# Kernel optimization log

Measured on AMD Instinct MI355X. Metric: run time of the kernel, lower is better.

## Reference

```python
import jax, jax.numpy as jnp
import numpy as np

HIDDEN = 100


def _mlp(x, w1, b1, w2, b2):
    # MLP(in, HIDDEN, output_size=out): Linear -> ReLU -> Linear
    return jnp.maximum(x @ w1 + b1, 0.0) @ w2 + b2


def _row_norm_mean(d):
    # mean_i sqrt(sum_j d_ij^2)  == torch.sqrt(einsum('ij,ij->i')).mean()
    return jnp.sqrt(jnp.einsum('ij,ij->i', d, d)).mean()


def _mismatch_1nn(mapped, target, idx):
    # torch_mapping_misclassified_1nn: cdist(mapped[idx], target), top-1 NN,
    # count non-integer distances at mismatched rows / len(idx).
    a = mapped[idx]                                     # [K, d]
    d2 = (jnp.sum(a * a, axis=1, keepdims=True)
          + jnp.sum(target * target, axis=1)[None, :]
          - 2.0 * a @ target.T)                         # [K, N]
    dist = jnp.sqrt(jnp.maximum(d2, 0.0))
    vals = jnp.min(dist, axis=1)                        # top-1 smallest value
    nn_inds = jnp.argmin(dist, axis=1)
    mismatch = (nn_inds != idx)
    count = (jnp.ceil(vals) - jnp.floor(vals)) * mismatch.astype(vals.dtype)
    return count.sum() / idx.shape[0]


def setup_inputs() -> dict:
    key = jax.random.key(0)
    ks = jax.random.split(key, 8)
    xN, yN, xd, yd, K = 25000, 25000, 100, 120, 8000
    s = 0.1
    return {
        'x_weight': jax.random.normal(ks[0], (xN, xd), jnp.float32) * s,
        'y_weight': jax.random.normal(ks[1], (yN, yd), jnp.float32) * s,
        'fx_w1': jax.random.normal(ks[2], (xd, HIDDEN), jnp.float32) * (1.0 / np.sqrt(xd)),
        'fx_b1': jnp.zeros((HIDDEN,), jnp.float32),
        'fx_w2': jax.random.normal(ks[3], (HIDDEN, yd), jnp.float32) * (1.0 / np.sqrt(HIDDEN)),
        'fx_b2': jnp.zeros((yd,), jnp.float32),
        'gy_w1': jax.random.normal(ks[4], (yd, HIDDEN), jnp.float32) * (1.0 / np.sqrt(yd)),
        'gy_b1': jnp.zeros((HIDDEN,), jnp.float32),
        'gy_w2': jax.random.normal(ks[5], (HIDDEN, xd), jnp.float32) * (1.0 / np.sqrt(HIDDEN)),
        'gy_b2': jnp.zeros((xd,), jnp.float32),
        'index_map': jax.random.randint(ks[6], (K, 2), 0, min(xN, yN), jnp.int64 if jax.config.jax_enable_x64 else jnp.int32),
    }


def reference(x_weight, y_weight, fx_w1, fx_b1, fx_w2, fx_b2,
              gy_w1, gy_b1, gy_w2, gy_b2, index_map):
    x_mapped = _mlp(x_weight, fx_w1, fx_b1, fx_w2, fx_b2)   # fx(x_emb)  [xN, yd]
    y_mapped = _mlp(y_weight, gy_w1, gy_b1, gy_w2, gy_b2)   # gy(y_emb)  [yN, xd]

    # cycle losses
    x_rt = _mlp(x_mapped, gy_w1, gy_b1, gy_w2, gy_b2)
    cycle_fx = _row_norm_mean(x_rt - x_weight)
    y_rt = _mlp(y_mapped, fx_w1, fx_b1, fx_w2, fx_b2)
    cycle_gy = _row_norm_mean(y_rt - y_weight)

    x_intersect = index_map[:, 0]
    y_intersect = index_map[:, 1]

    # supervised alignment losses
    sup_x = _row_norm_mean(x_mapped[x_intersect] - y_weight[y_intersect])
    sup_y = _row_norm_mean(y_mapped[y_intersect] - x_weight[x_intersect])

    # 1-NN mismatch losses (the cdist + top-1 hot spots)
    fx_mismatch = _mismatch_1nn(x_mapped, y_weight, x_intersect)
    gy_mismatch = _mismatch_1nn(y_mapped, x_weight, y_intersect)

    return cycle_fx + cycle_gy + sup_x + fx_mismatch + sup_y + gy_mismatch
```

## Files before the change

### kernel.cpp

```cpp
#include <hip/hip_runtime.h>
#include <hip/hip_bf16.h>
#include <math.h>

#define HIDDEN 100

typedef __attribute__((ext_vector_type(8))) short bf16x8;
typedef __attribute__((ext_vector_type(4))) float f32x4;

__device__ inline unsigned short f2bf(float v) {
    union { float f; unsigned u; } x; x.f = v;
    unsigned r = x.u + 0x7fff + ((x.u >> 16) & 1);
    return (unsigned short)(r >> 16);
}

constexpr int NPTS  = 25000;
constexpr int KPAIR = 8000;
constexpr int NC    = 28;
constexpr int CHUNK = 896;
constexpr int NPAD  = NC * CHUNK;
constexpr int HS    = 136;
constexpr int NB_SUP = 2000;
constexpr int GM     = (NPTS + 31) / 32;
constexpr int NB_MLP = 2 * GM;
constexpr int PREP_B = (2 * NPAD) / 4;

__global__ __launch_bounds__(256) void prep_kernel(
    const float* __restrict__ YW, float* __restrict__ tny, unsigned short* __restrict__ ybf,
    const float* __restrict__ XW, float* __restrict__ tnx, unsigned short* __restrict__ xbf,
    const float* __restrict__ W1, unsigned short* __restrict__ P1,
    const float* __restrict__ W2, unsigned short* __restrict__ P2,
    const float* __restrict__ W3, unsigned short* __restrict__ P3,
    const float* __restrict__ W4, unsigned short* __restrict__ P4,
    int N)
{
    const int ln = threadIdx.x & 63;
    if (blockIdx.x < PREP_B) {
        const int gw = blockIdx.x * 4 + (threadIdx.x >> 6);
        const int isY = (gw < NPAD);
        const int r = isY ? gw : gw - NPAD;
        const int D = isY ? 120 : 100;
        unsigned short* dst = (isY ? ybf : xbf) + (size_t)r * 128;
        if (r < N) {
            const float* src = (isY ? YW : XW) + (size_t)r * D;
            const float v0 = (ln < D) ? src[ln] : 0.f;
            const float v1 = (ln + 64 < D) ? src[ln + 64] : 0.f;
            float s = fmaf(v0, v0, v1 * v1);
            #pragma unroll
            for (int o = 1; o < 64; o <<= 1) s += __shfl_xor(s, o);
            if (ln == 0) (isY ? tny : tnx)[r] = s;
            dst[ln] = f2bf(v0);
            dst[ln + 64] = (ln == 63) ? f2bf(s) : f2bf(v1);
        } else {
            dst[ln] = 0;
            dst[ln + 64] = (ln == 63) ? f2bf(1e30f) : (unsigned short)0;
        }
        return;
    }
    int b = (blockIdx.x - PREP_B) * 4 + (threadIdx.x >> 6);
    if (b >= 116) return;
    const float* W; unsigned short* P; int DK, DN, NT;
    if (b < 28)      {          W = W1; P = P1; DK = 100; DN = 100; NT = 7; }
    else if (b < 60) { b -= 28; W = W2; P = P2; DK = 100; DN = 120; NT = 8; }
    else if (b < 88) { b -= 60; W = W3; P = P3; DK = 120; DN = 100; NT = 7; }
    else             { b -= 88; W = W4; P = P4; DK = 100; DN = 100; NT = 7; }
    const int kt = b / NT, nt = b - kt * NT;
    const int n  = nt * 16 + (ln & 15);
    const int k0 = kt * 32 + (ln >> 4) * 8;
    unsigned short* dst = P + ((size_t)(kt * NT + nt) * 64 + ln) * 8;
    #pragma unroll
    for (int j = 0; j < 8; j++) {
        const int k = k0 + j;
        const float f = (k < DK && n < DN) ? W[k * DN + n] : 0.f;
        dst[j] = f2bf(f);
    }
}

template<int NT>
__device__ inline void run_stage(const bf16x8 af[4], const unsigned short* __restrict__ WP,
                                 int ln, f32x4 acc[NT])
{
    #pragma unroll
    for (int nt = 0; nt < NT; nt++) acc[nt] = (f32x4){0.f, 0.f, 0.f, 0.f};
    #pragma unroll
    for (int kt = 0; kt < 4; kt++) {
        #pragma unroll
        for (int nt = 0; nt < NT; nt++) {
            const bf16x8 wf = *reinterpret_cast<const bf16x8*>(WP + ((size_t)(kt * NT + nt) * 64 + ln) * 8);
            acc[nt] = __builtin_amdgcn_mfma_f32_16x16x32_bf16(af[kt], wf, acc[nt], 0, 0, 0);
        }
    }
}

template<int NT, int DN, bool RELU>
__device__ inline void pack_h(const f32x4 acc[NT], const float* __restrict__ B,
                              unsigned short* __restrict__ Hs, int col, int quad)
{
    #pragma unroll
    for (int nt = 0; nt < NT; nt++) {
        const int n = nt * 16 + col;
        const float b = (n < DN) ? B[n] : 0.f;
        #pragma unroll
        for (int r = 0; r < 4; r++) {
            float v = acc[nt][r] + b;
            if (RELU) v = fmaxf(v, 0.f);
            Hs[(quad * 4 + r) * HS + n] = f2bf(v);
        }
    }
}

template<int NT, int DN>
__device__ inline void store_pack(const f32x4 acc[NT], const float* __restrict__ B,
                                  float* __restrict__ Y, unsigned short* __restrict__ Hs,
                                  int rowbase, int col, int quad, int N)
{
    #pragma unroll
    for (int nt = 0; nt < NT; nt++) {
        const int n = nt * 16 + col;
        const float b = (n < DN) ? B[n] : 0.f;
        #pragma unroll
        for (int r = 0; r < 4; r++) {
            const float v = acc[nt][r] + b;
            const int row = rowbase + quad * 4 + r;
            if (n < DN && row < N) Y[(size_t)row * DN + n] = v;
            Hs[(quad * 4 + r) * HS + n] = f2bf(v);
        }
    }
}

__device__ inline void load_haf(const unsigned short* __restrict__ Hs, int col, int quad,
                                bf16x8 af[4])
{
    const unsigned short* p = Hs + col * HS + quad * 8;
    #pragma unroll
    for (int kt = 0; kt < 4; kt++)
        af[kt] = *reinterpret_cast<const bf16x8*>(p + kt * 32);
}

template<int NT, int DN>
__device__ inline float norm_stage(const f32x4 acc[NT], const float* __restrict__ B,
                                   const float* __restrict__ REF,
                                   int rowbase, int col, int quad, int N)
{
    float ra[4] = {0.f, 0.f, 0.f, 0.f};
    #pragma unroll
    for (int nt = 0; nt < NT; nt++) {
        const int n = nt * 16 + col;
        if (n < DN) {
            const float b = B[n];
            #pragma unroll
            for (int r = 0; r < 4; r++) {
                const int row = rowbase + quad * 4 + r;
                if (row < N) {
                    const float d = acc[nt][r] + b - REF[(size_t)row * DN + n];
                    ra[r] = fmaf(d, d, ra[r]);
                }
            }
        }
    }
    #pragma unroll
    for (int o = 1; o < 16; o <<= 1) {
        #pragma unroll
        for (int r = 0; r < 4; r++) ra[r] += __shfl_xor(ra[r], o);
    }
    float s = 0.f;
    if (col == 0) {
        #pragma unroll
        for (int r = 0; r < 4; r++)
            if (rowbase + quad * 4 + r < N) s += sqrtf(ra[r]);
    }
    return s;
}

template<int DIN, int DMID, int NT2, int NTF>
__global__ __launch_bounds__(128) void mlp_fused(
    const unsigned short* __restrict__ Xbf,
    const float* __restrict__ XREF,
    const unsigned short* __restrict__ WP1, const float* __restrict__ B1,
    const unsigned short* __restrict__ WP2, const float* __restrict__ B2,
    const unsigned short* __restrict__ WP3, const float* __restrict__ B3,
    const unsigned short* __restrict__ WP4, const float* __restrict__ B4,
    float* __restrict__ Y,
    float* __restrict__ part, int N)
{
    __shared__ unsigned short H[2][16 * HS];
    __shared__ float bred[8];

    const int tid = threadIdx.x;
    const int wv = tid >> 6, ln = tid & 63;
    const int col = ln & 15, quad = ln >> 4;
    const int rowbase = blockIdx.x * 32 + wv * 16;

    {
        unsigned* Hz = reinterpret_cast<unsigned*>(H[wv]);
        for (int i = ln; i < 16 * HS / 2; i += 64) Hz[i] = 0u;
    }

    bf16x8 af[4];
    {
        const int r = min(rowbase + col, N - 1);
        const unsigned short* ap = Xbf + (size_t)r * 128 + quad * 8;
        #pragma unroll
        for (int kt = 0; kt < 4; kt++) af[kt] = *reinterpret_cast<const bf16x8*>(ap + kt * 32);
    }

    f32x4 accA[7];
    run_stage<7>(af, WP1, ln, accA);
    pack_h<7, HIDDEN, true>(accA, B1, H[wv], col, quad);
    load_haf(H[wv], col, quad, af);

    f32x4 accB[NT2];
    run_stage<NT2>(af, WP2, ln, accB);
    store_pack<NT2, DMID>(accB, B2, Y, H[wv], rowbase, col, quad, N);
    load_haf(H[wv], col, quad, af);

    run_stage<7>(af, WP3, ln, accA);
    pack_h<7, HIDDEN, true>(accA, B3, H[wv], col, quad);
    load_haf(H[wv], col, quad, af);

    f32x4 accC[NTF];
    run_stage<NTF>(af, WP4, ln, accC);
    const float s = norm_stage<NTF, DIN>(accC, B4, XREF, rowbase, col, quad, N);

    if (col == 0) bred[wv * 4 + quad] = s;
    __syncthreads();
    if (tid == 0) {
        float t = 0.f;
        #pragma unroll
        for (int i = 0; i < 8; i++) t += bred[i];
        part[blockIdx.x] = t;
    }
}

__global__ __launch_bounds__(256) void sup_gather(
    const float* __restrict__ xm, const float* __restrict__ ym,
    const float* __restrict__ xw, const float* __restrict__ yw,
    const int* __restrict__ im, int K, float* __restrict__ part,
    unsigned short* __restrict__ axf, unsigned short* __restrict__ ayf)
{
    const int gw = (int)((blockIdx.x * 256 + threadIdx.x) >> 6);
    const int ln = threadIdx.x & 63;
    const int wv = threadIdx.x >> 6;
    float cnt = 0.f;
    if (gw < K) {
        const int xi = im[2 * gw], yi = im[2 * gw + 1];
        const float* a = xm + (size_t)xi * 120;
        const float* b = yw + (size_t)yi * 120;
        const float a0 = a[ln];
        const float a1 = (ln + 64 < 120) ? a[ln + 64] : 0.f;
        float s1 = 0.f;
        { const float d0 = a0 - b[ln]; s1 = d0 * d0; }
        if (ln + 64 < 120) { const float d1 = a1 - b[ln + 64]; s1 = fmaf(d1, d1, s1); }
        unsigned short* pax = axf + (size_t)gw * 128;
        pax[ln] = f2bf(-2.f * a0);
        pax[ln + 64] = (ln == 63) ? f2bf(1.f) : ((ln + 64 < 120) ? f2bf(-2.f * a1) : (unsigned short)0);

        const float* c = ym + (size_t)yi * 100;
        const float* e = xw + (size_t)xi * 100;
        const float c0 = c[ln];
        const float c1 = (ln + 64 < 100) ? c[ln + 64] : 0.f;
        float s2 = 0.f;
        { const float d0 = c0 - e[ln]; s2 = d0 * d0; }
        if (ln + 64 < 100) { const float d1 = c1 - e[ln + 64]; s2 = fmaf(d1, d1, s2); }
        unsigned short* pay = ayf + (size_t)gw * 128;
        pay[ln] = f2bf(-2.f * c0);
        pay[ln + 64] = (ln == 63) ? f2bf(1.f) : ((ln + 64 < 100) ? f2bf(-2.f * c1) : (unsigned short)0);

        #pragma unroll
        for (int o = 32; o > 0; o >>= 1) { s1 += __shfl_down(s1, o); s2 += __shfl_down(s2, o); }
        if (ln == 0) cnt = sqrtf(s1) + sqrtf(s2);
    }
    __shared__ float wsum[4];
    if (ln == 0) wsum[wv] = cnt;
    __syncthreads();
    if (threadIdx.x == 0)
        part[blockIdx.x] = wsum[0] + wsum[1] + wsum[2] + wsum[3];
}

__device__ inline void stage_tile(const unsigned short* __restrict__ T, int jbase,
                                  unsigned char* smem, int buf, int wv, int ln)
{
    #pragma unroll
    for (int h = 0; h < 2; h++) {
        const int c = h * 256 + wv * 64 + ln;
        const int r = c >> 4;
        const int gc = (c & 15) ^ (r & 15);
        const unsigned short* g = T + ((size_t)(jbase + r) << 7) + gc * 8;
        unsigned char* l = smem + buf * 8192 + h * 4096 + wv * 1024;
        __builtin_amdgcn_global_load_lds(
            (const __attribute__((address_space(1))) void*)g,
            (__attribute__((address_space(3))) void*)l, 16, 0, 0);
    }
}

__global__ __launch_bounds__(256, 3) void nn_mfma(
    const unsigned short* __restrict__ A0, const unsigned short* __restrict__ T0,
    float* __restrict__ pm0, int* __restrict__ pi0,
    const unsigned short* __restrict__ A1, const unsigned short* __restrict__ T1,
    float* __restrict__ pm1, int* __restrict__ pi1,
    int K)
{
    __shared__ __align__(16) unsigned char smem[17408];
    float (*rm)[64][17] = reinterpret_cast<float(*)[64][17]>(smem);

    const unsigned short* A = blockIdx.z ? A1 : A0;
    const unsigned short* T = blockIdx.z ? T1 : T0;
    float* pmin = blockIdx.z ? pm1 : pm0;
    int*   pidx = blockIdx.z ? pi1 : pi0;

    const int tid = threadIdx.x;
    const int wv = tid >> 6, ln = tid & 63;
    const int col = ln & 15, quad = ln >> 4;
    const int k0 = blockIdx.x * 256;
    const int jstart = blockIdx.y * CHUNK;
    constexpr int NTILES = CHUNK / 32;

    bf16x8 afrag[4][4];
    #pragma unroll
    for (int t = 0; t < 4; t++) {
        const int ar = min(k0 + wv * 64 + t * 16 + col, K - 1);
        const unsigned short* ab = A + (size_t)ar * 128 + quad * 8;
        #pragma unroll
        for (int s = 0; s < 4; s++)
            afrag[t][s] = *reinterpret_cast<const bf16x8*>(ab + s * 32);
    }

    float m[4][4];
    #pragma unroll
    for (int t = 0; t < 4; t++)
        #pragma unroll
        for (int r = 0; r < 4; r++) m[t][r] = __builtin_inff();

    stage_tile(T, jstart, smem, 0, wv, ln);
    __syncthreads();

    for (int ti = 0; ti < NTILES; ti++) {
        const int cur = ti & 1;
        if (ti + 1 < NTILES)
            stage_tile(T, jstart + (ti + 1) * 32, smem, cur ^ 1, wv, ln);

        const unsigned short* base = (const unsigned short*)(smem + cur * 8192);
        const unsigned lowbase = (unsigned)((jstart + ti * 32) >> 4);
        #pragma unroll
        for (int sub = 0; sub < 2; sub++) {
            bf16x8 bfr[4];
            const int rr = sub * 16 + col;
            #pragma unroll
            for (int s = 0; s < 4; s++) {
                const int ch = rr * 16 + ((quad + s * 4) ^ col);
                bfr[s] = *reinterpret_cast<const bf16x8*>(base + ch * 8);
            }
            const unsigned low = lowbase + sub;
            #pragma unroll
            for (int t = 0; t < 4; t++) {
                f32x4 acc = {0.f, 0.f, 0.f, 0.f};
                #pragma unroll
                for (int s = 0; s < 4; s++)
                    acc = __builtin_amdgcn_mfma_f32_16x16x32_bf16(afrag[t][s], bfr[s], acc, 0, 0, 0);
                #pragma unroll
                for (int r = 0; r < 4; r++) {
                    const unsigned u = (__float_as_uint(acc[r]) & 0xFFFFF800u) | low;
                    m[t][r] = fminf(m[t][r], __uint_as_float(u));
                }
            }
        }
        __syncthreads();
    }

    #pragma unroll
    for (int t = 0; t < 4; t++)
        #pragma unroll
        for (int r = 0; r < 4; r++)
            rm[wv][t * 16 + quad * 4 + r][col] = m[t][r];
    __syncthreads();

    const int k = k0 + tid;
    if (k < K) {
        const int w = tid >> 6, rr = tid & 63;
        float best = rm[w][rr][0];
        int bc = 0;
        #pragma unroll
        for (int c = 1; c < 16; c++) {
            const float v = rm[w][rr][c];
            if (v < best) { best = v; bc = c; }
        }
        const int j = (int)(((__float_as_uint(best) & 0x7FFu) << 4) | (unsigned)bc);
        pmin[(size_t)k * NC + blockIdx.y] = best;
        pidx[(size_t)k * NC + blockIdx.y] = j;
    }
}

__global__ __launch_bounds__(256) void finish_all(
    const int* __restrict__ im,
    const float* __restrict__ pm0, const int* __restrict__ pi0,
    const float* __restrict__ pm1, const int* __restrict__ pi1,
    const float* __restrict__ part_sup, const float* __restrict__ part_mlp,
    int K, float* __restrict__ out, float inv_k, float inv_n)
{
    const int gid = blockIdx.x * 256 + threadIdx.x;
    const int stride = gridDim.x * 256;
    float local = 0.f;

    for (int p = gid; p < 2 * K; p += stride) {
        const int dir = (p >= K);
        const int kk = dir ? p - K : p;
        const float* pm = dir ? pm1 : pm0;
        const int*   pi = dir ? pi1 : pi0;
        float best = __builtin_inff();
        int bi = 0x7fffffff;
        #pragma unroll
        for (int c = 0; c < NC; c++) {
            const float v = pm[(size_t)kk * NC + c];
            const int  ii = pi[(size_t)kk * NC + c];
            if (v < best || (v == best && ii < bi)) { best = v; bi = ii; }
        }
        if (bi != im[2 * kk + dir]) local += inv_k;
    }
    for (int i = gid; i < NB_SUP; i += stride) local += part_sup[i] * inv_k;
    for (int i = gid; i < NB_MLP; i += stride) local += part_mlp[i] * inv_n;

    #pragma unroll
    for (int o = 32; o > 0; o >>= 1) local += __shfl_down(local, o);
    __shared__ float wsum[4];
    if ((threadIdx.x & 63) == 0) wsum[threadIdx.x >> 6] = local;
    __syncthreads();
    if (threadIdx.x == 0) {
        const float t = wsum[0] + wsum[1] + wsum[2] + wsum[3];
        if (t != 0.f) atomicAdd(out, t);
    }
}

extern "C" void kernel_launch(void* const* d_in, const int* in_sizes, int n_in,
                              void* d_out, int out_size, void* d_ws, size_t ws_size,
                              hipStream_t stream)
{
    const float* xw    = (const float*)d_in[0];
    const float* yw    = (const float*)d_in[1];
    const float* fx_w1 = (const float*)d_in[2];
    const float* fx_b1 = (const float*)d_in[3];
    const float* fx_w2 = (const float*)d_in[4];
    const float* fx_b2 = (const float*)d_in[5];
    const float* gy_w1 = (const float*)d_in[6];
    const float* gy_b1 = (const float*)d_in[7];
    const float* gy_w2 = (const float*)d_in[8];
    const float* gy_b2 = (const float*)d_in[9];
    const int*   imap  = (const int*)d_in[10];
    float* out = (float*)d_out;
    float* ws  = (float*)d_ws;

    constexpr int N = NPTS, K = KPAIR;

    float* xm      = ws;
    float* ym      = xm + (size_t)N * 120;
    float* tn_y    = ym + (size_t)N * 100;
    float* tn_x    = tn_y + N;
    float* pmin_fx = tn_x + N;
    int*   pidx_fx = (int*)(pmin_fx + (size_t)K * NC);
    float* pmin_gy = (float*)(pidx_fx + (size_t)K * NC);
    int*   pidx_gy = (int*)(pmin_gy + (size_t)K * NC);
    unsigned short* ybf = (unsigned short*)(pidx_gy + (size_t)K * NC);
    unsigned short* xbf = ybf + (size_t)NPAD * 128;
    unsigned short* axf = xbf + (size_t)NPAD * 128;
    unsigned short* ayf = axf + (size_t)K * 128;
    unsigned short* wp_fx1 = ayf + (size_t)K * 128;
    unsigned short* wp_fx2 = wp_fx1 + 28 * 512;
    unsigned short* wp_gy1 = wp_fx2 + 32 * 512;
    unsigned short* wp_gy2 = wp_gy1 + 28 * 512;
    float* part_sup = (float*)(wp_gy2 + 28 * 512);
    float* part_mlp = part_sup + NB_SUP;

    hipMemsetAsync(d_out, 0, sizeof(float), stream);

    prep_kernel<<<PREP_B + 29, 256, 0, stream>>>(
        yw, tn_y, ybf, xw, tn_x, xbf,
        fx_w1, wp_fx1, fx_w2, wp_fx2, gy_w1, wp_gy1, gy_w2, wp_gy2, N);

    mlp_fused<100, 120, 8, 7><<<GM, 128, 0, stream>>>(
        xbf, xw, wp_fx1, fx_b1, wp_fx2, fx_b2, wp_gy1, gy_b1, wp_gy2, gy_b2,
        xm, part_mlp, N);
    mlp_fused<120, 100, 7, 8><<<GM, 128, 0, stream>>>(
        ybf, yw, wp_gy1, gy_b1, wp_gy2, gy_b2, wp_fx1, fx_b1, wp_fx2, fx_b2,
        ym, part_mlp + GM, N);

    sup_gather<<<NB_SUP, 256, 0, stream>>>(xm, ym, xw, yw, imap, K, part_sup, axf, ayf);

    dim3 g1((K + 255) / 256, NC, 2);
    nn_mfma<<<g1, 256, 0, stream>>>(axf, ybf, pmin_fx, pidx_fx,
                                    ayf, xbf, pmin_gy, pidx_gy, K);

    finish_all<<<64, 256, 0, stream>>>(
        imap, pmin_fx, pidx_fx, pmin_gy, pidx_gy, part_sup, part_mlp,
        K, out, 1.f / K, 1.f / N);
}
```

Measured before the change: 237.7 us.

## Merge both MLP launches into one kernel and stage 64 rows per NN step

The two mlp_fused launches become one mlp_both kernel that picks the direction from the block index. This removes a launch boundary and lets blocks from both directions run concurrently. Separately, the NN kernel now double-buffers 64-row target tiles instead of 32, which halves the number of barriers per chunk. The cost is shared memory per block rising from 17 KB to 32 KB, which may reduce occupancy below the 3 blocks the launch bounds ask for.

```diff
diff --git a/kernel.cpp b/kernel.cpp
--- a/kernel.cpp
+++ b/kernel.cpp
@@ -172,23 +172,21 @@
 }
 
 template<int DIN, int DMID, int NT2, int NTF>
-__global__ __launch_bounds__(128) void mlp_fused(
+__device__ __forceinline__ void mlp_chain(
+    int bid,
     const unsigned short* __restrict__ Xbf,
     const float* __restrict__ XREF,
     const unsigned short* __restrict__ WP1, const float* __restrict__ B1,
     const unsigned short* __restrict__ WP2, const float* __restrict__ B2,
     const unsigned short* __restrict__ WP3, const float* __restrict__ B3,
     const unsigned short* __restrict__ WP4, const float* __restrict__ B4,
-    float* __restrict__ Y,
-    float* __restrict__ part, int N)
-{
-    __shared__ unsigned short H[2][16 * HS];
-    __shared__ float bred[8];
-
+    float* __restrict__ Y, float* __restrict__ part, int N,
+    unsigned short (*H)[16 * HS], float* bred)
+{
     const int tid = threadIdx.x;
     const int wv = tid >> 6, ln = tid & 63;
     const int col = ln & 15, quad = ln >> 4;
-    const int rowbase = blockIdx.x * 32 + wv * 16;
+    const int rowbase = bid * 32 + wv * 16;
 
     {
         unsigned* Hz = reinterpret_cast<unsigned*>(H[wv]);
@@ -227,7 +225,30 @@
         float t = 0.f;
         #pragma unroll
         for (int i = 0; i < 8; i++) t += bred[i];
-        part[blockIdx.x] = t;
+        part[bid] = t;
+    }
+}
+
+__global__ __launch_bounds__(128) void mlp_both(
+    const unsigned short* __restrict__ xbf, const float* __restrict__ xw,
+    const unsigned short* __restrict__ ybf, const float* __restrict__ yw,
+    const unsigned short* __restrict__ wp_fx1, const float* __restrict__ fx_b1,
+    const unsigned short* __restrict__ wp_fx2, const float* __restrict__ fx_b2,
+    const unsigned short* __restrict__ wp_gy1, const float* __restrict__ gy_b1,
+    const unsigned short* __restrict__ wp_gy2, const float* __restrict__ gy_b2,
+    float* __restrict__ xm, float* __restrict__ ym,
+    float* __restrict__ part, int N)
+{
+    __shared__ unsigned short H[2][16 * HS];
+    __shared__ float bred[8];
+    if (blockIdx.x < GM) {
+        mlp_chain<100, 120, 8, 7>(blockIdx.x, xbf, xw,
+            wp_fx1, fx_b1, wp_fx2, fx_b2, wp_gy1, gy_b1, wp_gy2, gy_b2,
+            xm, part, N, H, bred);
+    } else {
+        mlp_chain<120, 100, 7, 8>(blockIdx.x - GM, ybf, yw,
+            wp_gy1, gy_b1, wp_gy2, gy_b2, wp_fx1, fx_b1, wp_fx2, fx_b2,
+            ym, part + GM, N, H, bred);
     }
 }
 
@@ -276,8 +297,8 @@
         part[blockIdx.x] = wsum[0] + wsum[1] + wsum[2] + wsum[3];
 }
 
-__device__ inline void stage_tile(const unsigned short* __restrict__ T, int jbase,
-                                  unsigned char* smem, int buf, int wv, int ln)
+__device__ inline void stage32(const unsigned short* __restrict__ T, int jbase,
+                               unsigned char* dst0, int wv, int ln)
 {
     #pragma unroll
     for (int h = 0; h < 2; h++) {
@@ -285,7 +306,7 @@
         const int r = c >> 4;
         const int gc = (c & 15) ^ (r & 15);
         const unsigned short* g = T + ((size_t)(jbase + r) << 7) + gc * 8;
-        unsigned char* l = smem + buf * 8192 + h * 4096 + wv * 1024;
+        unsigned char* l = dst0 + h * 4096 + wv * 1024;
         __builtin_amdgcn_global_load_lds(
             (const __attribute__((address_space(1))) void*)g,
             (__attribute__((address_space(3))) void*)l, 16, 0, 0);
@@ -299,7 +320,7 @@
     float* __restrict__ pm1, int* __restrict__ pi1,
     int K)
 {
-    __shared__ __align__(16) unsigned char smem[17408];
+    __shared__ __align__(16) unsigned char smem[32768];
     float (*rm)[64][17] = reinterpret_cast<float(*)[64][17]>(smem);
 
     const unsigned short* A = blockIdx.z ? A1 : A0;
@@ -312,7 +333,7 @@
     const int col = ln & 15, quad = ln >> 4;
     const int k0 = blockIdx.x * 256;
     const int jstart = blockIdx.y * CHUNK;
-    constexpr int NTILES = CHUNK / 32;
+    constexpr int NSTEPS = CHUNK / 64;
 
     bf16x8 afrag[4][4];
     #pragma unroll
@@ -330,36 +351,43 @@
         #pragma unroll
         for (int r = 0; r < 4; r++) m[t][r] = __builtin_inff();
 
-    stage_tile(T, jstart, smem, 0, wv, ln);
+    stage32(T, jstart,      smem,        wv, ln);
+    stage32(T, jstart + 32, smem + 8192, wv, ln);
     __syncthreads();
 
-    for (int ti = 0; ti < NTILES; ti++) {
+    for (int ti = 0; ti < NSTEPS; ti++) {
         const int cur = ti & 1;
-        if (ti + 1 < NTILES)
-            stage_tile(T, jstart + (ti + 1) * 32, smem, cur ^ 1, wv, ln);
-
-        const unsigned short* base = (const unsigned short*)(smem + cur * 8192);
-        const unsigned lowbase = (unsigned)((jstart + ti * 32) >> 4);
-        #pragma unroll
-        for (int sub = 0; sub < 2; sub++) {
-            bf16x8 bfr[4];
-            const int rr = sub * 16 + col;
+        if (ti + 1 < NSTEPS) {
+            const int jn = jstart + (ti + 1) * 64;
+            stage32(T, jn,      smem + (cur ^ 1) * 16384,        wv, ln);
+            stage32(T, jn + 32, smem + (cur ^ 1) * 16384 + 8192, wv, ln);
+        }
+
+        #pragma unroll
+        for (int h = 0; h < 2; h++) {
+            const unsigned short* base = (const unsigned short*)(smem + cur * 16384 + h * 8192);
+            const unsigned lowbase = (unsigned)((jstart + ti * 64 + h * 32) >> 4);
             #pragma unroll
-            for (int s = 0; s < 4; s++) {
-                const int ch = rr * 16 + ((quad + s * 4) ^ col);
-                bfr[s] = *reinterpret_cast<const bf16x8*>(base + ch * 8);
-            }
-            const unsigned low = lowbase + sub;
-            #pragma unroll
-            for (int t = 0; t < 4; t++) {
-                f32x4 acc = {0.f, 0.f, 0.f, 0.f};
+            for (int sub = 0; sub < 2; sub++) {
+                bf16x8 bfr[4];
+                const int rr = sub * 16 + col;
                 #pragma unroll
-                for (int s = 0; s < 4; s++)
-                    acc = __builtin_amdgcn_mfma_f32_16x16x32_bf16(afrag[t][s], bfr[s], acc, 0, 0, 0);
+                for (int s = 0; s < 4; s++) {
+                    const int ch = rr * 16 + ((quad + s * 4) ^ col);
+                    bfr[s] = *reinterpret_cast<const bf16x8*>(base + ch * 8);
+                }
+                const unsigned low = lowbase + sub;
                 #pragma unroll
-                for (int r = 0; r < 4; r++) {
-                    const unsigned u = (__float_as_uint(acc[r]) & 0xFFFFF800u) | low;
-                    m[t][r] = fminf(m[t][r], __uint_as_float(u));
+                for (int t = 0; t < 4; t++) {
+                    f32x4 acc = {0.f, 0.f, 0.f, 0.f};
+                    #pragma unroll
+                    for (int s = 0; s < 4; s++)
+                        acc = __builtin_amdgcn_mfma_f32_16x16x32_bf16(afrag[t][s], bfr[s], acc, 0, 0, 0);
+                    #pragma unroll
+                    for (int r = 0; r < 4; r++) {
+                        const unsigned u = (__float_as_uint(acc[r]) & 0xFFFFF800u) | low;
+                        m[t][r] = fminf(m[t][r], __uint_as_float(u));
+                    }
                 }
             }
         }
@@ -474,12 +502,10 @@
         yw, tn_y, ybf, xw, tn_x, xbf,
         fx_w1, wp_fx1, fx_w2, wp_fx2, gy_w1, wp_gy1, gy_w2, wp_gy2, N);
 
-    mlp_fused<100, 120, 8, 7><<<GM, 128, 0, stream>>>(
-        xbf, xw, wp_fx1, fx_b1, wp_fx2, fx_b2, wp_gy1, gy_b1, wp_gy2, gy_b2,
-        xm, part_mlp, N);
-    mlp_fused<120, 100, 7, 8><<<GM, 128, 0, stream>>>(
-        ybf, yw, wp_gy1, gy_b1, wp_gy2, gy_b2, wp_fx1, fx_b1, wp_fx2, fx_b2,
-        ym, part_mlp + GM, N);
+    mlp_both<<<2 * GM, 128, 0, stream>>>(
+        xbf, xw, ybf, yw,
+        wp_fx1, fx_b1, wp_fx2, fx_b2, wp_gy1, gy_b1, wp_gy2, gy_b2,
+        xm, ym, part_mlp, N);
 
     sup_gather<<<NB_SUP, 256, 0, stream>>>(xm, ym, xw, yw, imap, K, part_sup, axf, ayf);
 
```

Measured after the change: 220.1 us. 1.08x faster.
